# Kernel tuning notes

Hardware: AMD Instinct MI355X
Metric: run time of the kernel (lower is better)

## Reference

```python
import jax, jax.numpy as jnp
import numpy as np

B, T, C = 4, 1024, 512      # batch, seq_len, n_attn
H, TT, D = 1, 1024, 16      # n_head (forced to 1 by kv.view), ctx_len, head_size


def setup_inputs() -> dict:
    key = jax.random.key(0)
    ks = jax.random.split(key, 13)
    s = 0.02
    return {
        "x": jax.random.normal(ks[0], (B, T, C), jnp.float32),
        "time_w": 1.0 + 0.1 * jax.random.normal(ks[1], (H, TT), jnp.float32),
        "time_alpha": 1.0 + 0.1 * jax.random.normal(ks[2], (H, 1, TT), jnp.float32),
        "time_beta": 1.0 + 0.1 * jax.random.normal(ks[3], (H, TT, 1), jnp.float32),
        "time_gamma": 1.0 + 0.1 * jax.random.normal(ks[4], (TT, 1), jnp.float32),
        "Wk": s * jax.random.normal(ks[5], (D, C), jnp.float32),
        "bk": jnp.zeros((D,), jnp.float32),
        "Wv": s * jax.random.normal(ks[6], (D, C), jnp.float32),
        "bv": jnp.zeros((D,), jnp.float32),
        "Wr": s * jax.random.normal(ks[7], (D, C), jnp.float32),
        "br": jnp.zeros((D,), jnp.float32),
        "Wo": s * jax.random.normal(ks[8], (64, D), jnp.float32),
        "bo": jnp.zeros((64,), jnp.float32),
    }


def reference(x, time_w, time_alpha, time_beta, time_gamma,
              Wk, bk, Wv, bv, Wr, br, Wo, bo):
    Tq = x.shape[1]
    # --- Toeplitz decay-matrix build (pad / tile / reshape trick) ---
    w = jnp.pad(time_w, ((0, 0), (0, TT)))                    # [H, 2TT]
    w = jnp.tile(w, (1, TT))[:, :-TT]                         # [H, 2TT*TT - TT]
    w = w.reshape(-1, TT, 2 * TT - 1)[:, :, TT - 1:]          # [H, TT, TT]
    w = w[:, :Tq, :Tq] * time_alpha[:, :, :Tq] * time_beta[:, :Tq, :]  # [H, T, T]
    # --- time shift on first half of channels (ZeroPad2d((0,0,1,-1))) ---
    half = x.shape[-1] // 2
    xs = jnp.pad(x[:, :, :half], ((0, 0), (1, 0), (0, 0)))[:, :-1]   # shift right by 1
    xx = jnp.concatenate([xs, x[:, :, half:]], axis=-1)              # [B, T, C]
    # --- k / v / r projections ---
    k = jnp.exp(jnp.clip(xx @ Wk.T + bk, -60.0, 30.0))        # [B, T, D]
    v = xx @ Wv.T + bv                                        # [B, T, D]
    r = xx @ Wr.T + br                                        # [B, T, D]
    sum_k = jnp.cumsum(k, axis=1)                             # [B, T, D]
    kv = k * v                                                # [B, T, D]
    # torch: kv.view(B,T,1,D).transpose(1,2) -> [B,1,T,D]; einsum 'htu,bthd->bhud'
    # broadcasts w's h=1 against kv's time axis and kv's t=1 against w's t axis:
    #   wkv[b,h,u,d] = (sum_t w[0,t,u]) * kv[b,h(time),d]
    w_sum = jnp.sum(w, axis=1)[0]                             # [T] over u
    wkv_full = w_sum[None, None, :, None] * kv[:, :, None, :] # [B, T, T, D]
    wkv = jnp.mean(wkv_full, axis=1)                          # mean over h -> [B, T, D]
    rwkv = r * wkv / (sum_k + 1e-8)                           # [B, T, D]
    out = (rwkv @ Wo.T + bo) * time_gamma[:Tq, :]             # [B, T, 64]
    return out
```

## Files before the change

### kernel.cpp

```cpp
#include <hip/hip_runtime.h>
#include <hip/hip_bf16.h>

typedef __hip_bfloat16 bf16;


__device__ __forceinline__ float ldf(const void* p, int f, long idx) {
    if (f == 0) return ((const float*)p)[idx];
    if (f == 1) {
        unsigned int u = ((unsigned int)((const unsigned short*)p)[idx]) << 16;
        float r; __builtin_memcpy(&r, &u, 4); return r;
    }
    return 0.f;
}

__device__ __forceinline__ float4 ld4(const void* p, int f, long idx) {
    if (f == 0) return ((const float4*)p)[idx >> 2];
    if (f == 1) {
        const unsigned short* sp = (const unsigned short*)p + idx;
        unsigned int u0 = ((unsigned int)sp[0]) << 16;
        unsigned int u1 = ((unsigned int)sp[1]) << 16;
        unsigned int u2 = ((unsigned int)sp[2]) << 16;
        unsigned int u3 = ((unsigned int)sp[3]) << 16;
        float4 r;
        __builtin_memcpy(&r.x, &u0, 4); __builtin_memcpy(&r.y, &u1, 4);
        __builtin_memcpy(&r.z, &u2, 4); __builtin_memcpy(&r.w, &u3, 4);
        return r;
    }
    return make_float4(0.f, 0.f, 0.f, 0.f);
}

__device__ __forceinline__ void sniff13(const void* const* ps, const int* ns,
                                        int tid, unsigned* mall, int* sf) {
    unsigned m = 0;
    for (int t = tid; t < 13 * 64; t += 256) {
        int p = t >> 6, j = t & 63;
        int n16 = ns[p] < 64 ? ns[p] : 64;
        if (j < n16) {
            unsigned short v = ((const unsigned short*)ps[p])[j];
            if (v != 0) m |= (1u << p);
        }
    }
    for (int t = tid; t < 13 * 32; t += 256) {
        int p = t >> 5, jp = t & 31;
        int n16 = ns[p] < 64 ? ns[p] : 64; int npair = n16 >> 1;
        if (jp < npair) {
            const unsigned short* u = (const unsigned short*)ps[p];
            unsigned short lo = u[2 * jp], hi = u[2 * jp + 1];
            int elo = (lo >> 7) & 0xFF, ehi = (hi >> 7) & 0xFF;
            bool lo_ok = (elo >= 64 && elo <= 190) || lo == 0;
            bool hi_ok = (ehi >= 64 && ehi <= 190) || hi == 0;
            if (!(lo_ok && hi_ok)) m |= (1u << (16 + p));
        }
    }
    #pragma unroll
    for (int off = 1; off < 64; off <<= 1) m |= __shfl_xor(m, off);
    if (tid == 0) *mall = 0;
    __syncthreads();
    if ((tid & 63) == 0) atomicOr(mall, m);
    __syncthreads();
    unsigned mm = *mall;
    if (tid < 13) {
        int f;
        if (!((mm >> tid) & 1)) f = 2;
        else f = ((mm >> (16 + tid)) & 1) ? 0 : 1;
        sf[tid] = f;
    }
    __syncthreads();
}

__device__ __forceinline__ float ldbias(const void* bk, const void* bv,
                                        const void* br, const int* sf, int o2) {
    if (o2 < 16) return ldf(bk, sf[6], o2);
    if (o2 < 32) return ldf(bv, sf[8], o2 - 16);
    if (o2 < 48) return ldf(br, sf[10], o2 - 32);
    return 0.f;
}

__global__ __launch_bounds__(256) void proj_kernel(
    const void* x, const void* tw, const void* alpha, const void* beta,
    const void* gamma, const void* Wk, const void* bk, const void* Wv,
    const void* bv, const void* Wr, const void* br, const void* Wo,
    const void* bo,
    int n0, int n1, int n2, int n3, int n4, int n5, int n6, int n7,
    int n8, int n9, int n10, int n11, int n12,
    float* __restrict__ k_ws, float* __restrict__ r_ws,
    float* __restrict__ blkS, float* __restrict__ blkKV,
    float* __restrict__ w_sum, int* __restrict__ flags)
{
    __shared__ float xs[8 * 512];
    __shared__ float red[16 * 8 * 64];
    __shared__ float kred[128], kvred[128];
    __shared__ float wsred[4];
    __shared__ int sf[16];
    __shared__ unsigned mall;
    int tid = threadIdx.x;
    const void* ps[13] = {x,tw,alpha,beta,gamma,Wk,bk,Wv,bv,Wr,br,Wo,bo};
    int ns[13] = {n0,n1,n2,n3,n4,n5,n6,n7,n8,n9,n10,n11,n12};
    sniff13(ps, ns, tid, &mall, sf);

    if (blockIdx.x == 0 && tid < 14) {
        if (tid == 13) {
            int any16 = 0;
            for (int j = 0; j < 13; ++j) if (sf[j] == 1) any16 = 1;
            flags[13] = any16;
        } else {
            flags[tid] = sf[tid];
        }
    }

    int row0 = blockIdx.x * 8;
    int b = row0 >> 10;
    int lt0 = row0 & 1023;
    int fx = sf[0];

    if (fx == 1) {
        const unsigned short* xp = (const unsigned short*)x;
        #pragma unroll
        for (int j = 0; j < 4; ++j) {
            int v = tid + 256 * j;
            int el = v * 4;
            int r = el >> 9, c = el & 511;
            int lt = lt0 + r - ((c < 256) ? 1 : 0);
            float4 f;
            if (lt < 0) f = make_float4(0.f, 0.f, 0.f, 0.f);
            else {
                const unsigned short* sp = xp + ((long)(b * 1024 + lt) * 512 + c);
                unsigned int u0 = ((unsigned int)sp[0]) << 16;
                unsigned int u1 = ((unsigned int)sp[1]) << 16;
                unsigned int u2 = ((unsigned int)sp[2]) << 16;
                unsigned int u3 = ((unsigned int)sp[3]) << 16;
                __builtin_memcpy(&f.x, &u0, 4); __builtin_memcpy(&f.y, &u1, 4);
                __builtin_memcpy(&f.z, &u2, 4); __builtin_memcpy(&f.w, &u3, 4);
            }
            reinterpret_cast<float4*>(xs)[v] = f;
        }
    } else {
        const float* xp = (const float*)x;
        #pragma unroll
        for (int j = 0; j < 4; ++j) {
            int v = tid + 256 * j;
            int el = v * 4;
            int r = el >> 9, c = el & 511;
            int lt = lt0 + r - ((c < 256) ? 1 : 0);
            float4 f;
            if (lt < 0) f = make_float4(0.f, 0.f, 0.f, 0.f);
            else f = *reinterpret_cast<const float4*>(xp + ((long)(b * 1024 + lt) * 512 + c));
            reinterpret_cast<float4*>(xs)[v] = f;
        }
    }
    __syncthreads();

    int o4 = tid & 15, cc = tid >> 4;
    const float4* xs4 = reinterpret_cast<const float4*>(xs);
    float a0[8], a1[8], a2[8], a3[8];
    #pragma unroll
    for (int r = 0; r < 8; ++r) { a0[r] = a1[r] = a2[r] = a3[r] = 0.f; }

    bool fastW = (sf[5] == 0) && (sf[7] == 0) && (sf[9] == 0);
    if (fastW) {
        if (o4 < 12) {
            const float* Wp = (o4 < 4) ? (const float*)Wk
                            : (o4 < 8) ? (const float*)Wv : (const float*)Wr;
            int rbase = (o4 & 3) * 4;
            const float4* Wq = reinterpret_cast<const float4*>(Wp);
            #pragma unroll
            for (int q = 0; q < 8; ++q) {
                int cq = cc * 8 + q;
                float4 w0 = Wq[(rbase + 0) * 128 + cq];
                float4 w1 = Wq[(rbase + 1) * 128 + cq];
                float4 w2 = Wq[(rbase + 2) * 128 + cq];
                float4 w3 = Wq[(rbase + 3) * 128 + cq];
                #pragma unroll
                for (int r = 0; r < 8; ++r) {
                    float4 x4 = xs4[r * 128 + cq];
                    a0[r] += x4.x * w0.x + x4.y * w0.y + x4.z * w0.z + x4.w * w0.w;
                    a1[r] += x4.x * w1.x + x4.y * w1.y + x4.z * w1.z + x4.w * w1.w;
                    a2[r] += x4.x * w2.x + x4.y * w2.y + x4.z * w2.z + x4.w * w2.w;
                    a3[r] += x4.x * w3.x + x4.y * w3.y + x4.z * w3.z + x4.w * w3.w;
                }
            }
        }
    } else {
        const void* Wp; int fw; int rbase;
        if (o4 < 4)       { Wp = Wk; fw = sf[5]; rbase = o4 * 4; }
        else if (o4 < 8)  { Wp = Wv; fw = sf[7]; rbase = (o4 - 4) * 4; }
        else if (o4 < 12) { Wp = Wr; fw = sf[9]; rbase = (o4 - 8) * 4; }
        else              { Wp = Wk; fw = 2;     rbase = 0; }
        #pragma unroll
        for (int q = 0; q < 8; ++q) {
            int cq = cc * 8 + q;
            float4 w0 = ld4(Wp, fw, (long)(rbase + 0) * 512 + cq * 4);
            float4 w1 = ld4(Wp, fw, (long)(rbase + 1) * 512 + cq * 4);
            float4 w2 = ld4(Wp, fw, (long)(rbase + 2) * 512 + cq * 4);
            float4 w3 = ld4(Wp, fw, (long)(rbase + 3) * 512 + cq * 4);
            #pragma unroll
            for (int r = 0; r < 8; ++r) {
                float4 x4 = xs4[r * 128 + cq];
                a0[r] += x4.x * w0.x + x4.y * w0.y + x4.z * w0.z + x4.w * w0.w;
                a1[r] += x4.x * w1.x + x4.y * w1.y + x4.z * w1.z + x4.w * w1.w;
                a2[r] += x4.x * w2.x + x4.y * w2.y + x4.z * w2.z + x4.w * w2.w;
                a3[r] += x4.x * w3.x + x4.y * w3.y + x4.z * w3.z + x4.w * w3.w;
            }
        }
    }
    float4* red4 = reinterpret_cast<float4*>(red);
    #pragma unroll
    for (int r = 0; r < 8; ++r)
        red4[(cc * 8 + r) * 16 + o4] = make_float4(a0[r], a1[r], a2[r], a3[r]);
    __syncthreads();

    #pragma unroll
    for (int it = 0; it < 2; ++it) {
        int idx = tid + 256 * it;
        int o2 = idx & 63, r2 = idx >> 6;
        float s = ldbias(bk, bv, br, sf, o2);
        #pragma unroll
        for (int cc2 = 0; cc2 < 16; ++cc2)
            s += red[(cc2 * 8 + r2) * 64 + o2];
        long a = (long)(lt0 + r2) * 64 + b * 16 + (o2 & 15);
        if (o2 < 16) {
            k_ws[a] = expf(fminf(fmaxf(s, -60.f), 30.f));
        } else if (o2 < 32) {
            int d = o2 - 16;
            float sk = ldbias(bk, bv, br, sf, d);
            #pragma unroll
            for (int cc2 = 0; cc2 < 16; ++cc2)
                sk += red[(cc2 * 8 + r2) * 64 + d];
            float kk = expf(fminf(fmaxf(sk, -60.f), 30.f));
            kred[d * 8 + r2] = kk;
            kvred[d * 8 + r2] = kk * s;
        } else if (o2 < 48) {
            r_ws[a] = s;
        }
    }
    __syncthreads();
    if (tid < 16) {
        float sk = 0.f, skv = 0.f;
        #pragma unroll
        for (int r = 0; r < 8; ++r) { sk += kred[tid * 8 + r]; skv += kvred[tid * 8 + r]; }
        blkS[(long)blockIdx.x * 16 + tid] = sk;
        blkKV[(long)blockIdx.x * 16 + tid] = skv;
    }

    {
        int g = tid >> 7, l = tid & 127;
        int u = blockIdx.x * 2 + g;
        int n = 1024 - u;
        int ftw = sf[1], fbe = sf[3];
        float acc = 0.f;
        for (int s = l; s < n; s += 128)
            acc += ldf(tw, ftw, 1023 - s) * ldf(beta, fbe, u + s);
        #pragma unroll
        for (int off = 32; off > 0; off >>= 1) acc += __shfl_xor(acc, off);
        if ((tid & 63) == 0) wsred[tid >> 6] = acc;
        __syncthreads();
        if ((tid & 127) == 0)
            w_sum[u] = (wsred[g * 2] + wsred[g * 2 + 1]) * ldf(alpha, sf[2], u);
    }
}

__global__ __launch_bounds__(256) void out_kernel(
    const void* gamma, const void* Wo, const void* bo,
    const float* __restrict__ k_ws, const float* __restrict__ r_ws,
    const float* __restrict__ blkS, const float* __restrict__ blkKV,
    const float* __restrict__ w_sum, const int* __restrict__ flags,
    void* __restrict__ out)
{
    __shared__ float redc[256], redk[256];
    __shared__ float cums[16], kvm[16], kk8[8][16], rr8[8][16], rw[8][16];
    __shared__ int sfl[16];
    int tid = threadIdx.x;
    if (tid < 16) sfl[tid] = flags[tid];

    int row0 = blockIdx.x * 8;
    int b = row0 >> 10;
    int t0 = row0 & 1023;
    int nch = t0 >> 3;
    long base = (long)b * 16;

    {
        int d = tid & 15, lane = tid >> 4;
        float pc = 0.f, pk = 0.f;
        for (int ch = lane; ch < nch; ch += 16) pc += blkS[((long)b * 128 + ch) * 16 + d];
        for (int ch = lane; ch < 128; ch += 16) pk += blkKV[((long)b * 128 + ch) * 16 + d];
        redc[tid] = pc; redk[tid] = pk;
    }
    if (tid < 128) {
        int rl = tid >> 4, dd = tid & 15;
        kk8[rl][dd] = k_ws[(long)(t0 + rl) * 64 + base + dd];
    } else {
        int tt = tid - 128; int rl = tt >> 4, dd = tt & 15;
        rr8[rl][dd] = r_ws[(long)(t0 + rl) * 64 + base + dd];
    }
    __syncthreads();
    if (tid < 16) {
        float c = 0.f, kv = 0.f;
        #pragma unroll
        for (int ln = 0; ln < 16; ++ln) { c += redc[ln * 16 + tid]; kv += redk[ln * 16 + tid]; }
        cums[tid] = c;
        kvm[tid] = kv * (1.0f / 1024.0f);
    }
    __syncthreads();

    if (tid < 128) {
        int rl = tid >> 4, o = tid & 15;
        float ck = cums[o];
        for (int i = 0; i <= rl; ++i) ck += kk8[i][o];
        rw[rl][o] = rr8[rl][o] * w_sum[t0 + rl] * kvm[o] / (ck + 1e-8f);
    }
    __syncthreads();

    int fWo = sfl[11], fbo = sfl[12], fga = sfl[4], any16 = sfl[13];
    #pragma unroll
    for (int it = 0; it < 2; ++it) {
        int idx = tid + 256 * it;
        int rl = idx >> 6, o = idx & 63;
        int t = t0 + rl;
        float acc = ldf(bo, fbo, o);
        #pragma unroll
        for (int j = 0; j < 4; ++j) {
            float4 w = ld4(Wo, fWo, (long)o * 16 + 4 * j);
            acc += rw[rl][4 * j + 0] * w.x + rw[rl][4 * j + 1] * w.y +
                   rw[rl][4 * j + 2] * w.z + rw[rl][4 * j + 3] * w.w;
        }
        float val = acc * ldf(gamma, fga, t);
        long oa = (long)(row0 + rl) * 64 + o;
        if (any16) ((bf16*)out)[oa] = __float2bfloat16(val);
        else       ((float*)out)[oa] = val;
    }
}

extern "C" void kernel_launch(void* const* d_in, const int* in_sizes, int n_in,
                              void* d_out, int out_size, void* d_ws, size_t ws_size,
                              hipStream_t stream) {
    const void* x     = d_in[0];
    const void* tw    = d_in[1];
    const void* alpha = d_in[2];
    const void* beta  = d_in[3];
    const void* gamma = d_in[4];
    const void* Wk    = d_in[5];
    const void* bk    = d_in[6];
    const void* Wv    = d_in[7];
    const void* bv    = d_in[8];
    const void* Wr    = d_in[9];
    const void* br    = d_in[10];
    const void* Wo    = d_in[11];
    const void* bo    = d_in[12];

    float* ws    = (float*)d_ws;
    float* k_ws  = ws;
    float* r_ws  = ws + 65536;
    float* blkS  = ws + 131072;
    float* blkKV = ws + 139264;
    float* w_sum = ws + 147456;
    int*   flags = (int*)(ws + 148480);

    proj_kernel<<<512, 256, 0, stream>>>(
        x, tw, alpha, beta, gamma, Wk, bk, Wv, bv, Wr, br, Wo, bo,
        in_sizes[0], in_sizes[1], in_sizes[2], in_sizes[3], in_sizes[4],
        in_sizes[5], in_sizes[6], in_sizes[7], in_sizes[8], in_sizes[9],
        in_sizes[10], in_sizes[11], in_sizes[12],
        k_ws, r_ws, blkS, blkKV, w_sum, flags);
    out_kernel<<<512, 256, 0, stream>>>(
        gamma, Wo, bo, k_ws, r_ws, blkS, blkKV, w_sum, flags, (void*)d_out);
}
```

Baseline: 113.2 us.

## Restructure projection GEMV to wave-per-output-rows with shuffle reductions

```diff
diff --git a/kernel.cpp b/kernel.cpp
--- a/kernel.cpp
+++ b/kernel.cpp
@@ -88,7 +88,7 @@
     float* __restrict__ w_sum, int* __restrict__ flags)
 {
     __shared__ float xs[8 * 512];
-    __shared__ float red[16 * 8 * 64];
+    __shared__ float sred[8][48];
     __shared__ float kred[128], kvred[128];
     __shared__ float wsred[4];
     __shared__ int sf[16];
@@ -150,87 +150,88 @@
     }
     __syncthreads();
 
-    int o4 = tid & 15, cc = tid >> 4;
+    int lane = tid & 63, wv = tid >> 6;
     const float4* xs4 = reinterpret_cast<const float4*>(xs);
-    float a0[8], a1[8], a2[8], a3[8];
+    const void* Wm[3] = {Wk, Wv, Wr};
+    int fwm[3] = {sf[5], sf[7], sf[9]};
     #pragma unroll
-    for (int r = 0; r < 8; ++r) { a0[r] = a1[r] = a2[r] = a3[r] = 0.f; }
-
-    bool fastW = (sf[5] == 0) && (sf[7] == 0) && (sf[9] == 0);
-    if (fastW) {
-        if (o4 < 12) {
-            const float* Wp = (o4 < 4) ? (const float*)Wk
-                            : (o4 < 8) ? (const float*)Wv : (const float*)Wr;
-            int rbase = (o4 & 3) * 4;
+    for (int m = 0; m < 3; ++m) {
+        const void* Wp = Wm[m]; int fw = fwm[m];
+        float acc[4][8];
+        #pragma unroll
+        for (int oi = 0; oi < 4; ++oi)
+            #pragma unroll
+            for (int r = 0; r < 8; ++r) acc[oi][r] = 0.f;
+
+        if (fw == 0) {
             const float4* Wq = reinterpret_cast<const float4*>(Wp);
             #pragma unroll
-            for (int q = 0; q < 8; ++q) {
-                int cq = cc * 8 + q;
-                float4 w0 = Wq[(rbase + 0) * 128 + cq];
-                float4 w1 = Wq[(rbase + 1) * 128 + cq];
-                float4 w2 = Wq[(rbase + 2) * 128 + cq];
-                float4 w3 = Wq[(rbase + 3) * 128 + cq];
+            for (int j = 0; j < 2; ++j) {
+                int c4 = lane + 64 * j;
+                float4 xr[8];
                 #pragma unroll
-                for (int r = 0; r < 8; ++r) {
-                    float4 x4 = xs4[r * 128 + cq];
-                    a0[r] += x4.x * w0.x + x4.y * w0.y + x4.z * w0.z + x4.w * w0.w;
-                    a1[r] += x4.x * w1.x + x4.y * w1.y + x4.z * w1.z + x4.w * w1.w;
-                    a2[r] += x4.x * w2.x + x4.y * w2.y + x4.z * w2.z + x4.w * w2.w;
-                    a3[r] += x4.x * w3.x + x4.y * w3.y + x4.z * w3.z + x4.w * w3.w;
+                for (int r = 0; r < 8; ++r) xr[r] = xs4[r * 128 + c4];
+                #pragma unroll
+                for (int oi = 0; oi < 4; ++oi) {
+                    int row = wv * 4 + oi;
+                    float4 wq = Wq[row * 128 + c4];
+                    #pragma unroll
+                    for (int r = 0; r < 8; ++r)
+                        acc[oi][r] += xr[r].x * wq.x + xr[r].y * wq.y +
+                                      xr[r].z * wq.z + xr[r].w * wq.w;
                 }
             }
-        }
-    } else {
-        const void* Wp; int fw; int rbase;
-        if (o4 < 4)       { Wp = Wk; fw = sf[5]; rbase = o4 * 4; }
-        else if (o4 < 8)  { Wp = Wv; fw = sf[7]; rbase = (o4 - 4) * 4; }
-        else if (o4 < 12) { Wp = Wr; fw = sf[9]; rbase = (o4 - 8) * 4; }
-        else              { Wp = Wk; fw = 2;     rbase = 0; }
-        #pragma unroll
-        for (int q = 0; q < 8; ++q) {
-            int cq = cc * 8 + q;
-            float4 w0 = ld4(Wp, fw, (long)(rbase + 0) * 512 + cq * 4);
-            float4 w1 = ld4(Wp, fw, (long)(rbase + 1) * 512 + cq * 4);
-            float4 w2 = ld4(Wp, fw, (long)(rbase + 2) * 512 + cq * 4);
-            float4 w3 = ld4(Wp, fw, (long)(rbase + 3) * 512 + cq * 4);
+        } else {
+            #pragma unroll
+            for (int j = 0; j < 2; ++j) {
+                int c4 = lane + 64 * j;
+                float4 xr[8];
+                #pragma unroll
+                for (int r = 0; r < 8; ++r) xr[r] = xs4[r * 128 + c4];
+                #pragma unroll
+                for (int oi = 0; oi < 4; ++oi) {
+                    int row = wv * 4 + oi;
+                    float4 wq = ld4(Wp, fw, (long)row * 512 + c4 * 4);
+                    #pragma unroll
+                    for (int r = 0; r < 8; ++r)
+                        acc[oi][r] += xr[r].x * wq.x + xr[r].y * wq.y +
+                                      xr[r].z * wq.z + xr[r].w * wq.w;
+                }
+            }
+        }
+        #pragma unroll
+        for (int oi = 0; oi < 4; ++oi) {
             #pragma unroll
             for (int r = 0; r < 8; ++r) {
-                float4 x4 = xs4[r * 128 + cq];
-                a0[r] += x4.x * w0.x + x4.y * w0.y + x4.z * w0.z + x4.w * w0.w;
-                a1[r] += x4.x * w1.x + x4.y * w1.y + x4.z * w1.z + x4.w * w1.w;
-                a2[r] += x4.x * w2.x + x4.y * w2.y + x4.z * w2.z + x4.w * w2.w;
-                a3[r] += x4.x * w3.x + x4.y * w3.y + x4.z * w3.z + x4.w * w3.w;
-            }
-        }
-    }
-    float4* red4 = reinterpret_cast<float4*>(red);
-    #pragma unroll
-    for (int r = 0; r < 8; ++r)
-        red4[(cc * 8 + r) * 16 + o4] = make_float4(a0[r], a1[r], a2[r], a3[r]);
+                float a = acc[oi][r];
+                a += __shfl_xor(a, 1);  a += __shfl_xor(a, 2);
+                a += __shfl_xor(a, 4);  a += __shfl_xor(a, 8);
+                a += __shfl_xor(a, 16); a += __shfl_xor(a, 32);
+                if (lane == oi * 8 + r)
+                    sred[r][m * 16 + wv * 4 + oi] = a;
+            }
+        }
+    }
     __syncthreads();
 
     #pragma unroll
     for (int it = 0; it < 2; ++it) {
         int idx = tid + 256 * it;
         int o2 = idx & 63, r2 = idx >> 6;
-        float s = ldbias(bk, bv, br, sf, o2);
-        #pragma unroll
-        for (int cc2 = 0; cc2 < 16; ++cc2)
-            s += red[(cc2 * 8 + r2) * 64 + o2];
-        long a = (long)(lt0 + r2) * 64 + b * 16 + (o2 & 15);
-        if (o2 < 16) {
-            k_ws[a] = expf(fminf(fmaxf(s, -60.f), 30.f));
-        } else if (o2 < 32) {
-            int d = o2 - 16;
-            float sk = ldbias(bk, bv, br, sf, d);
-            #pragma unroll
-            for (int cc2 = 0; cc2 < 16; ++cc2)
-                sk += red[(cc2 * 8 + r2) * 64 + d];
-            float kk = expf(fminf(fmaxf(sk, -60.f), 30.f));
-            kred[d * 8 + r2] = kk;
-            kvred[d * 8 + r2] = kk * s;
-        } else if (o2 < 48) {
-            r_ws[a] = s;
+        if (o2 < 48) {
+            float s = ldbias(bk, bv, br, sf, o2) + sred[r2][o2];
+            long a = (long)(lt0 + r2) * 64 + b * 16 + (o2 & 15);
+            if (o2 < 16) {
+                k_ws[a] = expf(fminf(fmaxf(s, -60.f), 30.f));
+            } else if (o2 < 32) {
+                int d = o2 - 16;
+                float sk = ldbias(bk, bv, br, sf, d) + sred[r2][d];
+                float kk = expf(fminf(fmaxf(sk, -60.f), 30.f));
+                kred[d * 8 + r2] = kk;
+                kvred[d * 8 + r2] = kk * s;
+            } else {
+                r_ws[a] = s;
+            }
         }
     }
     __syncthreads();
@@ -311,22 +312,43 @@
     __syncthreads();
 
     int fWo = sfl[11], fbo = sfl[12], fga = sfl[4], any16 = sfl[13];
-    #pragma unroll
-    for (int it = 0; it < 2; ++it) {
-        int idx = tid + 256 * it;
-        int rl = idx >> 6, o = idx & 63;
-        int t = t0 + rl;
-        float acc = ldf(bo, fbo, o);
-        #pragma unroll
-        for (int j = 0; j < 4; ++j) {
-            float4 w = ld4(Wo, fWo, (long)o * 16 + 4 * j);
-            acc += rw[rl][4 * j + 0] * w.x + rw[rl][4 * j + 1] * w.y +
-                   rw[rl][4 * j + 2] * w.z + rw[rl][4 * j + 3] * w.w;
-        }
-        float val = acc * ldf(gamma, fga, t);
-        long oa = (long)(row0 + rl) * 64 + o;
-        if (any16) ((bf16*)out)[oa] = __float2bfloat16(val);
-        else       ((float*)out)[oa] = val;
+    if (fWo == 0) {
+        const float4* Wq = reinterpret_cast<const float4*>(Wo);
+        #pragma unroll
+        for (int it = 0; it < 2; ++it) {
+            int idx = tid + 256 * it;
+            int rl = idx >> 6, o = idx & 63;
+            int t = t0 + rl;
+            float acc = ldf(bo, fbo, o);
+            #pragma unroll
+            for (int j = 0; j < 4; ++j) {
+                float4 w = Wq[o * 4 + j];
+                acc += rw[rl][4 * j + 0] * w.x + rw[rl][4 * j + 1] * w.y +
+                       rw[rl][4 * j + 2] * w.z + rw[rl][4 * j + 3] * w.w;
+            }
+            float val = acc * ldf(gamma, fga, t);
+            long oa = (long)(row0 + rl) * 64 + o;
+            if (any16) ((bf16*)out)[oa] = __float2bfloat16(val);
+            else       ((float*)out)[oa] = val;
+        }
+    } else {
+        #pragma unroll
+        for (int it = 0; it < 2; ++it) {
+            int idx = tid + 256 * it;
+            int rl = idx >> 6, o = idx & 63;
+            int t = t0 + rl;
+            float acc = ldf(bo, fbo, o);
+            #pragma unroll
+            for (int j = 0; j < 4; ++j) {
+                float4 w = ld4(Wo, fWo, (long)o * 16 + 4 * j);
+                acc += rw[rl][4 * j + 0] * w.x + rw[rl][4 * j + 1] * w.y +
+                       rw[rl][4 * j + 2] * w.z + rw[rl][4 * j + 3] * w.w;
+            }
+            float val = acc * ldf(gamma, fga, t);
+            long oa = (long)(row0 + rl) * 64 + o;
+            if (any16) ((bf16*)out)[oa] = __float2bfloat16(val);
+            else       ((float*)out)[oa] = val;
+        }
     }
 }
 
```

Result: no change. 115.2 us (+1.8%).

## Stage projection weights through swizzled shared memory in column chunks

Applied to the files above, without the earlier changes.

```diff
diff --git a/kernel.cpp b/kernel.cpp
--- a/kernel.cpp
+++ b/kernel.cpp
@@ -68,14 +68,6 @@
     __syncthreads();
 }
 
-__device__ __forceinline__ float ldbias(const void* bk, const void* bv,
-                                        const void* br, const int* sf, int o2) {
-    if (o2 < 16) return ldf(bk, sf[6], o2);
-    if (o2 < 32) return ldf(bv, sf[8], o2 - 16);
-    if (o2 < 48) return ldf(br, sf[10], o2 - 32);
-    return 0.f;
-}
-
 __global__ __launch_bounds__(256) void proj_kernel(
     const void* x, const void* tw, const void* alpha, const void* beta,
     const void* gamma, const void* Wk, const void* bk, const void* Wv,
@@ -88,9 +80,8 @@
     float* __restrict__ w_sum, int* __restrict__ flags)
 {
     __shared__ float xs[8 * 512];
-    __shared__ float red[16 * 8 * 64];
-    __shared__ float kred[128], kvred[128];
-    __shared__ float wsred[4];
+    __shared__ float uni[8192];
+    __shared__ float kred[128], kvred[128], wsred[4];
     __shared__ int sf[16];
     __shared__ unsigned mall;
     int tid = threadIdx.x;
@@ -152,24 +143,43 @@
 
     int o4 = tid & 15, cc = tid >> 4;
     const float4* xs4 = reinterpret_cast<const float4*>(xs);
+    float4* wt4 = reinterpret_cast<float4*>(uni);
     float a0[8], a1[8], a2[8], a3[8];
     #pragma unroll
     for (int r = 0; r < 8; ++r) { a0[r] = a1[r] = a2[r] = a3[r] = 0.f; }
-
     bool fastW = (sf[5] == 0) && (sf[7] == 0) && (sf[9] == 0);
-    if (fastW) {
+
+    for (int ch = 0; ch < 4; ++ch) {
+        #pragma unroll
+        for (int i = 0; i < 6; ++i) {
+            int idx = tid + 256 * i;
+            int r = idx >> 5, c4 = idx & 31;
+            int col = ch * 128 + c4 * 4;
+            float4 w;
+            if (fastW) {
+                const float* Wp = (r < 16) ? (const float*)Wk
+                                : (r < 32) ? (const float*)Wv : (const float*)Wr;
+                w = *reinterpret_cast<const float4*>(Wp + (long)(r & 15) * 512 + col);
+            } else {
+                const void* Wp; int fw;
+                if (r < 16)      { Wp = Wk; fw = sf[5]; }
+                else if (r < 32) { Wp = Wv; fw = sf[7]; }
+                else             { Wp = Wr; fw = sf[9]; }
+                w = ld4(Wp, fw, (long)(r & 15) * 512 + col);
+            }
+            wt4[r * 32 + (c4 ^ ((r >> 2) & 7))] = w;
+        }
+        __syncthreads();
         if (o4 < 12) {
-            const float* Wp = (o4 < 4) ? (const float*)Wk
-                            : (o4 < 8) ? (const float*)Wv : (const float*)Wr;
-            int rbase = (o4 & 3) * 4;
-            const float4* Wq = reinterpret_cast<const float4*>(Wp);
             #pragma unroll
-            for (int q = 0; q < 8; ++q) {
-                int cq = cc * 8 + q;
-                float4 w0 = Wq[(rbase + 0) * 128 + cq];
-                float4 w1 = Wq[(rbase + 1) * 128 + cq];
-                float4 w2 = Wq[(rbase + 2) * 128 + cq];
-                float4 w3 = Wq[(rbase + 3) * 128 + cq];
+            for (int q = 0; q < 2; ++q) {
+                int cql = cc * 2 + q;
+                int cq = ch * 32 + cql;
+                int sw = cql ^ (o4 & 7);
+                float4 w0 = wt4[(o4 * 4 + 0) * 32 + sw];
+                float4 w1 = wt4[(o4 * 4 + 1) * 32 + sw];
+                float4 w2 = wt4[(o4 * 4 + 2) * 32 + sw];
+                float4 w3 = wt4[(o4 * 4 + 3) * 32 + sw];
                 #pragma unroll
                 for (int r = 0; r < 8; ++r) {
                     float4 x4 = xs4[r * 128 + cq];
@@ -180,57 +190,45 @@
                 }
             }
         }
-    } else {
-        const void* Wp; int fw; int rbase;
-        if (o4 < 4)       { Wp = Wk; fw = sf[5]; rbase = o4 * 4; }
-        else if (o4 < 8)  { Wp = Wv; fw = sf[7]; rbase = (o4 - 4) * 4; }
-        else if (o4 < 12) { Wp = Wr; fw = sf[9]; rbase = (o4 - 8) * 4; }
-        else              { Wp = Wk; fw = 2;     rbase = 0; }
-        #pragma unroll
-        for (int q = 0; q < 8; ++q) {
-            int cq = cc * 8 + q;
-            float4 w0 = ld4(Wp, fw, (long)(rbase + 0) * 512 + cq * 4);
-            float4 w1 = ld4(Wp, fw, (long)(rbase + 1) * 512 + cq * 4);
-            float4 w2 = ld4(Wp, fw, (long)(rbase + 2) * 512 + cq * 4);
-            float4 w3 = ld4(Wp, fw, (long)(rbase + 3) * 512 + cq * 4);
-            #pragma unroll
-            for (int r = 0; r < 8; ++r) {
-                float4 x4 = xs4[r * 128 + cq];
-                a0[r] += x4.x * w0.x + x4.y * w0.y + x4.z * w0.z + x4.w * w0.w;
-                a1[r] += x4.x * w1.x + x4.y * w1.y + x4.z * w1.z + x4.w * w1.w;
-                a2[r] += x4.x * w2.x + x4.y * w2.y + x4.z * w2.z + x4.w * w2.w;
-                a3[r] += x4.x * w3.x + x4.y * w3.y + x4.z * w3.z + x4.w * w3.w;
-            }
-        }
-    }
-    float4* red4 = reinterpret_cast<float4*>(red);
-    #pragma unroll
-    for (int r = 0; r < 8; ++r)
-        red4[(cc * 8 + r) * 16 + o4] = make_float4(a0[r], a1[r], a2[r], a3[r]);
-    __syncthreads();
-
+        __syncthreads();
+    }
+
+    float4* red4 = reinterpret_cast<float4*>(uni);
+    if (o4 < 12) {
+        #pragma unroll
+        for (int r = 0; r < 8; ++r)
+            red4[(cc * 8 + r) * 16 + o4] = make_float4(a0[r], a1[r], a2[r], a3[r]);
+    }
+    __syncthreads();
+
+    const float* red = uni;
     #pragma unroll
     for (int it = 0; it < 2; ++it) {
         int idx = tid + 256 * it;
         int o2 = idx & 63, r2 = idx >> 6;
-        float s = ldbias(bk, bv, br, sf, o2);
-        #pragma unroll
-        for (int cc2 = 0; cc2 < 16; ++cc2)
-            s += red[(cc2 * 8 + r2) * 64 + o2];
-        long a = (long)(lt0 + r2) * 64 + b * 16 + (o2 & 15);
-        if (o2 < 16) {
-            k_ws[a] = expf(fminf(fmaxf(s, -60.f), 30.f));
-        } else if (o2 < 32) {
-            int d = o2 - 16;
-            float sk = ldbias(bk, bv, br, sf, d);
+        if (o2 < 48) {
+            float S;
+            if (o2 < 16)      S = ldf(bk, sf[6], o2);
+            else if (o2 < 32) S = ldf(bv, sf[8], o2 - 16);
+            else              S = ldf(br, sf[10], o2 - 32);
             #pragma unroll
             for (int cc2 = 0; cc2 < 16; ++cc2)
-                sk += red[(cc2 * 8 + r2) * 64 + d];
-            float kk = expf(fminf(fmaxf(sk, -60.f), 30.f));
-            kred[d * 8 + r2] = kk;
-            kvred[d * 8 + r2] = kk * s;
-        } else if (o2 < 48) {
-            r_ws[a] = s;
+                S += red[(cc2 * 8 + r2) * 64 + o2];
+            long a = (long)(lt0 + r2) * 64 + b * 16 + (o2 & 15);
+            if (o2 < 16) {
+                k_ws[a] = expf(fminf(fmaxf(S, -60.f), 30.f));
+            } else if (o2 < 32) {
+                int d = o2 - 16;
+                float sk = ldf(bk, sf[6], d);
+                #pragma unroll
+                for (int cc2 = 0; cc2 < 16; ++cc2)
+                    sk += red[(cc2 * 8 + r2) * 64 + d];
+                float kk = expf(fminf(fmaxf(sk, -60.f), 30.f));
+                kred[d * 8 + r2] = kk;
+                kvred[d * 8 + r2] = kk * S;
+            } else {
+                r_ws[a] = S;
+            }
         }
     }
     __syncthreads();
@@ -311,22 +309,43 @@
     __syncthreads();
 
     int fWo = sfl[11], fbo = sfl[12], fga = sfl[4], any16 = sfl[13];
-    #pragma unroll
-    for (int it = 0; it < 2; ++it) {
-        int idx = tid + 256 * it;
-        int rl = idx >> 6, o = idx & 63;
-        int t = t0 + rl;
-        float acc = ldf(bo, fbo, o);
-        #pragma unroll
-        for (int j = 0; j < 4; ++j) {
-            float4 w = ld4(Wo, fWo, (long)o * 16 + 4 * j);
-            acc += rw[rl][4 * j + 0] * w.x + rw[rl][4 * j + 1] * w.y +
-                   rw[rl][4 * j + 2] * w.z + rw[rl][4 * j + 3] * w.w;
-        }
-        float val = acc * ldf(gamma, fga, t);
-        long oa = (long)(row0 + rl) * 64 + o;
-        if (any16) ((bf16*)out)[oa] = __float2bfloat16(val);
-        else       ((float*)out)[oa] = val;
+    if (fWo == 0) {
+        const float4* Wq = reinterpret_cast<const float4*>(Wo);
+        #pragma unroll
+        for (int it = 0; it < 2; ++it) {
+            int idx = tid + 256 * it;
+            int rl = idx >> 6, o = idx & 63;
+            int t = t0 + rl;
+            float acc = ldf(bo, fbo, o);
+            #pragma unroll
+            for (int j = 0; j < 4; ++j) {
+                float4 w = Wq[o * 4 + j];
+                acc += rw[rl][4 * j + 0] * w.x + rw[rl][4 * j + 1] * w.y +
+                       rw[rl][4 * j + 2] * w.z + rw[rl][4 * j + 3] * w.w;
+            }
+            float val = acc * ldf(gamma, fga, t);
+            long oa = (long)(row0 + rl) * 64 + o;
+            if (any16) ((bf16*)out)[oa] = __float2bfloat16(val);
+            else       ((float*)out)[oa] = val;
+        }
+    } else {
+        #pragma unroll
+        for (int it = 0; it < 2; ++it) {
+            int idx = tid + 256 * it;
+            int rl = idx >> 6, o = idx & 63;
+            int t = t0 + rl;
+            float acc = ldf(bo, fbo, o);
+            #pragma unroll
+            for (int j = 0; j < 4; ++j) {
+                float4 w = ld4(Wo, fWo, (long)o * 16 + 4 * j);
+                acc += rw[rl][4 * j + 0] * w.x + rw[rl][4 * j + 1] * w.y +
+                       rw[rl][4 * j + 2] * w.z + rw[rl][4 * j + 3] * w.w;
+            }
+            float val = acc * ldf(gamma, fga, t);
+            long oa = (long)(row0 + rl) * 64 + o;
+            if (any16) ((bf16*)out)[oa] = __float2bfloat16(val);
+            else       ((float*)out)[oa] = val;
+        }
     }
 }
 
```

Result: faster. 106.0 us (-6.3%).
